# Kernel optimization log

Hardware: AMD Instinct MI355X
Metric: run time of the kernel (lower is better)

## Reference

```python
import jax, jax.numpy as jnp
import numpy as np

D_MODEL = 256
N_HEAD = 4
LEN_Q, LEN_K, BATCH = 1024, 4096, 8


def setup_inputs() -> dict:
    key = jax.random.key(0)
    ks = jax.random.split(key, 10)
    s = 0.02  # small init scale (stands in for xavier)
    return {
        "tgt": jax.random.normal(ks[0], (LEN_Q, BATCH, D_MODEL), jnp.float32),
        "memory": jax.random.normal(ks[1], (LEN_K, BATCH, D_MODEL), jnp.float32),
        "pos": jax.random.normal(ks[2], (LEN_K, BATCH, D_MODEL), jnp.float32),
        "query_pos": jax.random.normal(ks[3], (LEN_Q, BATCH, D_MODEL), jnp.float32),
        # nn.Linear weights, torch layout [out, in]
        "Wq": jax.random.normal(ks[4], (N_HEAD * D_MODEL, D_MODEL), jnp.float32) * s,
        "Wk": jax.random.normal(ks[5], (N_HEAD * D_MODEL, D_MODEL), jnp.float32) * s,
        "Wv": jax.random.normal(ks[6], (N_HEAD * D_MODEL, D_MODEL), jnp.float32) * s,
        "Wfc": jax.random.normal(ks[7], (D_MODEL, N_HEAD * D_MODEL), jnp.float32) * s,
        "ln_g": jnp.ones((D_MODEL,), jnp.float32),
        "ln_b": jnp.zeros((D_MODEL,), jnp.float32),
    }


def _layernorm(x, g, b, eps=1e-5):
    mu = jnp.mean(x, axis=-1, keepdims=True)
    var = jnp.mean(jnp.square(x - mu), axis=-1, keepdims=True)
    return (x - mu) * jax.lax.rsqrt(var + eps) * g + b


def reference(tgt, memory, pos, query_pos, Wq, Wk, Wv, Wfc, ln_g, ln_b):
    H, D = N_HEAD, D_MODEL
    # seq-first -> batch-first  [B, L, D]
    q = jnp.swapaxes(tgt + query_pos, 0, 1)
    k = jnp.swapaxes(memory + pos, 0, 1)
    v = jnp.swapaxes(memory, 0, 1)
    # per-head projections: each head has full d_model width
    Wq_h = Wq.reshape(H, D, D)
    Wk_h = Wk.reshape(H, D, D)
    Wv_h = Wv.reshape(H, D, D)
    qh = jnp.einsum('bqd,hed->bhqe', q, Wq_h)  # [B,H,Lq,D]
    kh = jnp.einsum('bkd,hed->bhke', k, Wk_h)  # [B,H,Lk,D]
    vh = jnp.einsum('bkd,hed->bhke', v, Wv_h)  # [B,H,Lk,D]
    scale = 1.0 / jnp.sqrt(jnp.asarray(D, qh.dtype))
    attn_logits = jnp.einsum('bhqe,bhke->bhqk', qh * scale, kh)  # [B,H,Lq,Lk]
    attn = jax.nn.softmax(attn_logits, axis=-1)
    out = jnp.einsum('bhqk,bhke->bhqe', attn, vh)  # [B,H,Lq,D]
    # mean logits across heads (keepdim), as returned attention map
    attn_mean = jnp.mean(attn_logits, axis=1, keepdims=True)  # [B,1,Lq,Lk]
    # concat heads, fc projection
    out = jnp.swapaxes(out, 1, 2).reshape(out.shape[0], -1, H * D)  # [B,Lq,H*D]
    out = out @ Wfc.T  # [B,Lq,D]
    tgt2 = jnp.swapaxes(out, 0, 1)  # back to [Lq,B,D]
    # residual + LayerNorm (dropout=0.0)
    y = _layernorm(tgt + tgt2, ln_g, ln_b)
    return (y, attn_mean)
```

## Files before the change

### kernel.cpp

```cpp
#include <hip/hip_runtime.h>
#include <cstdint>
#include <cstddef>

#define LQ 1024
#define LK 4096
#define NBATCH 8
#define DM 256
#define NH 4

typedef __attribute__((ext_vector_type(8))) __bf16 bf16x8;
typedef __attribute__((ext_vector_type(4))) float f32x4;
typedef __attribute__((ext_vector_type(4))) unsigned int u32x4;
typedef __attribute__((ext_vector_type(4))) short s16x4;

__device__ __forceinline__ unsigned short f2bf(float f) {
  unsigned int u = __builtin_bit_cast(unsigned int, f);
  u += 0x7FFFu + ((u >> 16) & 1u);
  return (unsigned short)(u >> 16);
}
__device__ __forceinline__ unsigned pack2(float a, float b) {
  return (unsigned)f2bf(a) | ((unsigned)f2bf(b) << 16);
}
__device__ __forceinline__ bf16x8 ld_bf8(const unsigned short* p) {
  u32x4 u = *reinterpret_cast<const u32x4*>(p);
  return __builtin_bit_cast(bf16x8, u);
}
__device__ __forceinline__ f32x4 zero4() {
  f32x4 v; v.x = 0.f; v.y = 0.f; v.z = 0.f; v.w = 0.f; return v;
}

#define ASYNC16(ldsp, gp)                                                      \
  __builtin_amdgcn_global_load_lds(                                            \
      (const __attribute__((address_space(1))) unsigned int*)(gp),             \
      (__attribute__((address_space(3))) unsigned int*)(ldsp), 16, 0, 0)

__global__ void prep_add_kernel(const float* __restrict__ a,
                                const float* __restrict__ badd,
                                unsigned short* __restrict__ out,
                                int L, int n8) {
  int i = blockIdx.x * blockDim.x + threadIdx.x;
  if (i >= n8) return;
  int base = i * 8;
  int d = base & 255;
  int rest = base >> 8;
  int bb = rest & 7, l = rest >> 3;
  f32x4 x0 = *reinterpret_cast<const f32x4*>(a + base);
  f32x4 x1 = *reinterpret_cast<const f32x4*>(a + base + 4);
  if (badd) {
    f32x4 y0 = *reinterpret_cast<const f32x4*>(badd + base);
    f32x4 y1 = *reinterpret_cast<const f32x4*>(badd + base + 4);
    x0 += y0; x1 += y1;
  }
  u32x4 o;
  o.x = pack2(x0.x, x0.y); o.y = pack2(x0.z, x0.w);
  o.z = pack2(x1.x, x1.y); o.w = pack2(x1.z, x1.w);
  *reinterpret_cast<u32x4*>(out + (((size_t)bb * L + l) << 8) + d) = o;
}

__global__ void conv_bf16_kernel(const float* __restrict__ src,
                                 unsigned short* __restrict__ dst, int n8) {
  int i = blockIdx.x * blockDim.x + threadIdx.x;
  if (i >= n8) return;
  int base = i * 8;
  f32x4 x0 = *reinterpret_cast<const f32x4*>(src + base);
  f32x4 x1 = *reinterpret_cast<const f32x4*>(src + base + 4);
  u32x4 o;
  o.x = pack2(x0.x, x0.y); o.y = pack2(x0.z, x0.w);
  o.z = pack2(x1.x, x1.y); o.w = pack2(x1.z, x1.w);
  *reinterpret_cast<u32x4*>(dst + base) = o;
}

template <int OUT_MODE>
__global__ void __launch_bounds__(256)
gemm_nt_kernel(const unsigned short* __restrict__ A, int lda, long long sA,
               const unsigned short* __restrict__ B, int ldb, long long sB,
               void* __restrict__ Cv, int ldc, long long sC,
               int K, float alpha) {
  __shared__ __align__(16) unsigned short As[128 * 64];
  __shared__ __align__(16) unsigned short Bs[128 * 64];
  const int t = threadIdx.x;
  const int bm0 = blockIdx.y * 128;
  const int bn0 = blockIdx.x * 128;
  A += (size_t)blockIdx.z * sA + (size_t)bm0 * lda;
  B += (size_t)blockIdx.z * sB + (size_t)bn0 * ldb;
  const int lane = t & 63, w = t >> 6;
  const int wm = (w >> 1) * 64, wn = (w & 1) * 64;
  const int lr = lane & 15, quad = lane >> 4;
  const int srl = lane >> 3;
  const int sc = (lane & 7) ^ (srl & 7);

  f32x4 acc[4][4];
#pragma unroll
  for (int i = 0; i < 4; ++i)
#pragma unroll
    for (int j = 0; j < 4; ++j) acc[i][j] = zero4();

  for (int k0 = 0; k0 < K; k0 += 64) {
#pragma unroll
    for (int i = 0; i < 4; ++i) {
      int r0 = w * 32 + i * 8;
      ASYNC16(&As[r0 * 64], &A[(size_t)(r0 + srl) * lda + k0 + sc * 8]);
      ASYNC16(&Bs[r0 * 64], &B[(size_t)(r0 + srl) * ldb + k0 + sc * 8]);
    }
    __syncthreads();
#pragma unroll
    for (int ks = 0; ks < 2; ++ks) {
      bf16x8 af[4], bfv[4];
#pragma unroll
      for (int i = 0; i < 4; ++i) {
        int m = wm + i * 16 + lr;
        int pc = (ks * 4 + quad) ^ (lr & 7);
        af[i] = ld_bf8(&As[m * 64 + pc * 8]);
      }
#pragma unroll
      for (int j = 0; j < 4; ++j) {
        int n = wn + j * 16 + lr;
        int pc = (ks * 4 + quad) ^ (lr & 7);
        bfv[j] = ld_bf8(&Bs[n * 64 + pc * 8]);
      }
#pragma unroll
      for (int i = 0; i < 4; ++i)
#pragma unroll
        for (int j = 0; j < 4; ++j)
          acc[i][j] = __builtin_amdgcn_mfma_f32_16x16x32_bf16(af[i], bfv[j], acc[i][j], 0, 0, 0);
    }
    __syncthreads();
  }

  if (OUT_MODE == 0) {
    float* C = (float*)Cv + (size_t)blockIdx.z * sC;
#pragma unroll
    for (int i = 0; i < 4; ++i) {
      int m0 = bm0 + wm + i * 16 + quad * 4;
#pragma unroll
      for (int j = 0; j < 4; ++j) {
        int n = bn0 + wn + j * 16 + lr;
#pragma unroll
        for (int r = 0; r < 4; ++r)
          C[(size_t)(m0 + r) * ldc + n] = acc[i][j][r] * alpha;
      }
    }
  } else if (OUT_MODE == 1) {
    unsigned short* C = (unsigned short*)Cv + (size_t)blockIdx.z * sC;
#pragma unroll
    for (int i = 0; i < 4; ++i) {
      int m0 = bm0 + wm + i * 16 + quad * 4;
#pragma unroll
      for (int j = 0; j < 4; ++j) {
        int n = bn0 + wn + j * 16 + lr;
#pragma unroll
        for (int r = 0; r < 4; ++r)
          C[(size_t)(m0 + r) * ldc + n] = f2bf(acc[i][j][r] * alpha);
      }
    }
  } else {
    unsigned short* C = (unsigned short*)Cv;
#pragma unroll
    for (int i = 0; i < 4; ++i) {
      int m0 = bm0 + wm + i * 16 + quad * 4;
      int bb = m0 >> 12;
      int kp = m0 & 4095;
#pragma unroll
      for (int j = 0; j < 4; ++j) {
        int n = bn0 + wn + j * 16 + lr;
        s16x4 pk;
#pragma unroll
        for (int r = 0; r < 4; ++r) pk[r] = (short)f2bf(acc[i][j][r] * alpha);
        *reinterpret_cast<s16x4*>(&C[((size_t)(bb * 1024 + n)) * 4096 + kp]) = pk;
      }
    }
  }
}

__global__ void __launch_bounds__(256, 2)
attn_kernel(const unsigned short* __restrict__ Qg,
            const unsigned short* __restrict__ Kg,
            const unsigned short* __restrict__ VTg,
            unsigned short* __restrict__ Opart,
            float* __restrict__ lpart) {
  __shared__ __align__(16) unsigned short Kt[2][32 * 256];
  __shared__ __align__(16) unsigned short Vt[2][256 * 32];
  const int t = threadIdx.x;
  const int qt = blockIdx.x >> 1, ks = blockIdx.x & 1;
  const int h = blockIdx.y, b = blockIdx.z;
  const int lane = t & 63, w = t >> 6;
  const int lr = lane & 15, quad = lane >> 4;

  const unsigned short* Qrow0 =
      Qg + ((size_t)(b * 1024 + qt * 128 + w * 32 + lr)) * 1024 + h * 256;
  bf16x8 qf[2][8];
#pragma unroll
  for (int s = 0; s < 8; ++s) {
    qf[0][s] = ld_bf8(&Qrow0[s * 32 + quad * 8]);
    qf[1][s] = ld_bf8(&Qrow0[16 * 1024 + s * 32 + quad * 8]);
  }

  f32x4 Oacc[16][2];
#pragma unroll
  for (int m2 = 0; m2 < 16; ++m2) {
    Oacc[m2][0] = zero4();
    Oacc[m2][1] = zero4();
  }
  float lsum_r[2] = {0.f, 0.f};

  const unsigned short* Kb =
      Kg + ((size_t)(b * 4096 + ks * 2048)) * 1024 + h * 256;
  const unsigned short* Vb =
      VTg + ((size_t)(b * 1024 + h * 256)) * 4096 + ks * 2048;

  const int k_rsub = lane >> 5;
  const int k_chunk = lane & 31;
  const int v_rsub = lane >> 2;
  const int v_chunk = lane & 3;

#define ISSUE_TILE(kt, bufsel)                                                 \
  {                                                                            \
    _Pragma("unroll") for (int i = 0; i < 4; ++i) {                            \
      int r0 = w * 8 + i * 2;                                                  \
      int krow = r0 + k_rsub;                                                  \
      int kc = k_chunk ^ (krow & 7);                                           \
      ASYNC16(&Kt[bufsel][r0 * 256], &Kb[(size_t)((kt) + krow) * 1024 + kc * 8]); \
      int vr0 = (w * 4 + i) * 16;                                              \
      int ve = vr0 + v_rsub;                                                   \
      int vc = v_chunk ^ ((ve >> 1) & 3);                                      \
      ASYNC16(&Vt[bufsel][vr0 * 32], &Vb[(size_t)ve * 4096 + (kt) + vc * 8]);  \
    }                                                                          \
  }

  ISSUE_TILE(0, 0)
  __syncthreads();

  const int bpermA = (((quad & 1) * 32) + lr) * 4;
  const int bpermB = bpermA + 64;

  for (int kt = 0; kt < 2048; kt += 32) {
    const int pbuf = (kt >> 5) & 1;
    ISSUE_TILE(kt + 32, pbuf ^ 1)

    const unsigned short* Ktp = Kt[pbuf];
    const unsigned short* Vtp = Vt[pbuf];

    f32x4 S[2][2];
    S[0][0] = zero4(); S[0][1] = zero4();
    S[1][0] = zero4(); S[1][1] = zero4();
#pragma unroll
    for (int s = 0; s < 8; ++s) {
      int pc = ((s * 4 + quad) ^ (lr & 7)) * 8;
      bf16x8 kf0 = ld_bf8(&Ktp[lr * 256 + pc]);
      bf16x8 kf1 = ld_bf8(&Ktp[(16 + lr) * 256 + pc]);
      S[0][0] = __builtin_amdgcn_mfma_f32_16x16x32_bf16(kf0, qf[0][s], S[0][0], 0, 0, 0);
      S[0][1] = __builtin_amdgcn_mfma_f32_16x16x32_bf16(kf0, qf[1][s], S[0][1], 0, 0, 0);
      S[1][0] = __builtin_amdgcn_mfma_f32_16x16x32_bf16(kf1, qf[0][s], S[1][0], 0, 0, 0);
      S[1][1] = __builtin_amdgcn_mfma_f32_16x16x32_bf16(kf1, qf[1][s], S[1][1], 0, 0, 0);
    }

    unsigned pk[2][2][2];
#pragma unroll
    for (int mt = 0; mt < 2; ++mt)
#pragma unroll
      for (int nt = 0; nt < 2; ++nt) {
        float p0 = __expf(S[mt][nt][0]);
        float p1 = __expf(S[mt][nt][1]);
        float p2 = __expf(S[mt][nt][2]);
        float p3 = __expf(S[mt][nt][3]);
        lsum_r[nt] += (p0 + p1) + (p2 + p3);
        pk[mt][nt][0] = pack2(p0, p1);
        pk[mt][nt][1] = pack2(p2, p3);
      }

    bf16x8 pfrag[2];
#pragma unroll
    for (int nt = 0; nt < 2; ++nt) {
      u32x4 bfw;
#pragma unroll
      for (int w2 = 0; w2 < 2; ++w2) {
        int f0 = __builtin_amdgcn_ds_bpermute(bpermA, (int)pk[0][nt][w2]);
        int f1 = __builtin_amdgcn_ds_bpermute(bpermA, (int)pk[1][nt][w2]);
        bfw[w2] = (unsigned)(quad < 2 ? f0 : f1);
        int g0 = __builtin_amdgcn_ds_bpermute(bpermB, (int)pk[0][nt][w2]);
        int g1 = __builtin_amdgcn_ds_bpermute(bpermB, (int)pk[1][nt][w2]);
        bfw[2 + w2] = (unsigned)(quad < 2 ? g0 : g1);
      }
      pfrag[nt] = __builtin_bit_cast(bf16x8, bfw);
    }

#pragma unroll
    for (int m2 = 0; m2 < 16; ++m2) {
      bf16x8 vf = ld_bf8(&Vtp[(m2 * 16 + lr) * 32 + (quad ^ ((lr >> 1) & 3)) * 8]);
      Oacc[m2][0] = __builtin_amdgcn_mfma_f32_16x16x32_bf16(vf, pfrag[0], Oacc[m2][0], 0, 0, 0);
      Oacc[m2][1] = __builtin_amdgcn_mfma_f32_16x16x32_bf16(vf, pfrag[1], Oacc[m2][1], 0, 0, 0);
    }
    __syncthreads();
  }
#undef ISSUE_TILE

  const int pidx = b * 4 + h;
#pragma unroll
  for (int nt = 0; nt < 2; ++nt) {
    float l = lsum_r[nt];
    l += __shfl_xor(l, 16, 64);
    l += __shfl_xor(l, 32, 64);
    if (quad == 0)
      lpart[((size_t)(ks * 32 + pidx)) * 1024 + qt * 128 + w * 32 + nt * 16 + lr] = l;
  }

  const size_t base = ((size_t)(ks * 32 + pidx)) * 256 * 1024;
  const int qg0 = qt * 128 + w * 32 + lr;
#pragma unroll
  for (int m2 = 0; m2 < 16; ++m2) {
#pragma unroll
    for (int nt = 0; nt < 2; ++nt) {
#pragma unroll
      for (int r = 0; r < 4; ++r) {
        int e = m2 * 16 + quad * 4 + r;
        Opart[base + (size_t)e * 1024 + qg0 + nt * 16] = f2bf(Oacc[m2][nt][r]);
      }
    }
  }
}

__global__ void __launch_bounds__(256)
combine_kernel(const unsigned short* __restrict__ Opart,
               const float* __restrict__ lpart,
               unsigned short* __restrict__ Oall) {
  __shared__ float rl[64];
  __shared__ __align__(16) unsigned short T[64][264];
  const int t = threadIdx.x;
  const int qt = blockIdx.x, h = blockIdx.y, b = blockIdx.z;
  const int p = b * 4 + h;
  const int q0 = qt * 64;
  const size_t slabO = (size_t)32 * 256 * 1024;
  const size_t slabL = (size_t)32 * 1024;
  if (t < 64) {
    float la = lpart[(size_t)p * 1024 + q0 + t];
    float lb = lpart[slabL + (size_t)p * 1024 + q0 + t];
    rl[t] = 1.f / (la + lb);
  }
  __syncthreads();
  const int er = t >> 3, q8 = t & 7;
#pragma unroll
  for (int ei = 0; ei < 8; ++ei) {
    int e = ei * 32 + er;
    size_t idx = ((size_t)p * 256 + e) * 1024 + q0 + q8 * 8;
    u32x4 ua = *reinterpret_cast<const u32x4*>(&Opart[idx]);
    u32x4 ub = *reinterpret_cast<const u32x4*>(&Opart[slabO + idx]);
#pragma unroll
    for (int wd = 0; wd < 4; ++wd) {
      unsigned a = ((const unsigned*)&ua)[wd], bb2 = ((const unsigned*)&ub)[wd];
      float a0 = __builtin_bit_cast(float, a << 16);
      float a1 = __builtin_bit_cast(float, a & 0xFFFF0000u);
      float b0 = __builtin_bit_cast(float, bb2 << 16);
      float b1 = __builtin_bit_cast(float, bb2 & 0xFFFF0000u);
      int qA = q8 * 8 + wd * 2;
      T[qA + 0][e] = f2bf((a0 + b0) * rl[qA + 0]);
      T[qA + 1][e] = f2bf((a1 + b1) * rl[qA + 1]);
    }
  }
  __syncthreads();
  const int ql = t >> 2, ec = t & 3;
  const size_t orow = ((size_t)(b * 1024 + q0 + ql)) * 1024 + h * 256;
#pragma unroll
  for (int i = 0; i < 8; ++i) {
    int ch = ec * 8 + i;
    *reinterpret_cast<u32x4*>(&Oall[orow + ch * 8]) =
        *reinterpret_cast<const u32x4*>(&T[ql][ch * 8]);
  }
}

__global__ void __launch_bounds__(256)
fc_ln_kernel(const float* __restrict__ fc, const float* __restrict__ tgt,
             const float* __restrict__ g, const float* __restrict__ bb,
             float* __restrict__ y) {
  int row = blockIdx.x * 4 + (threadIdx.x >> 6);
  int lane = threadIdx.x & 63;
  int b = row >> 10, q = row & 1023;
  const float* fr = fc + (size_t)row * 256;
  const float* tr = tgt + ((size_t)(q * 8 + b)) * 256;
  float x[4];
  float s = 0.f, ss = 0.f;
#pragma unroll
  for (int e = 0; e < 4; ++e) {
    x[e] = fr[lane + e * 64] + tr[lane + e * 64];
    s += x[e];
    ss += x[e] * x[e];
  }
#pragma unroll
  for (int d = 1; d < 64; d <<= 1) {
    s += __shfl_xor(s, d, 64);
    ss += __shfl_xor(ss, d, 64);
  }
  float mu = s * (1.f / 256.f);
  float var = ss * (1.f / 256.f) - mu * mu;
  float rs = rsqrtf(var + 1e-5f);
  float* yr = y + ((size_t)(q * 8 + b)) * 256;
#pragma unroll
  for (int e = 0; e < 4; ++e)
    yr[lane + e * 64] = (x[e] - mu) * rs * g[lane + e * 64] + bb[lane + e * 64];
}

extern "C" void kernel_launch(void* const* d_in, const int* in_sizes, int n_in,
                              void* d_out, int out_size, void* d_ws, size_t ws_size,
                              hipStream_t stream) {
  (void)in_sizes; (void)n_in; (void)out_size; (void)ws_size;
  const float* tgt    = (const float*)d_in[0];
  const float* memory = (const float*)d_in[1];
  const float* pos    = (const float*)d_in[2];
  const float* qpos   = (const float*)d_in[3];
  const float* Wq     = (const float*)d_in[4];
  const float* Wk     = (const float*)d_in[5];
  const float* Wv     = (const float*)d_in[6];
  const float* Wfc    = (const float*)d_in[7];
  const float* lng    = (const float*)d_in[8];
  const float* lnb    = (const float*)d_in[9];
  float* out = (float*)d_out;

  char* ws = (char*)d_ws;
  const size_t MB = 1024 * 1024;
  unsigned short* Wq_b  = (unsigned short*)(ws + 0);
  unsigned short* Wk_b  = (unsigned short*)(ws + 512 * 1024);
  unsigned short* Wv_b  = (unsigned short*)(ws + 1 * MB);
  unsigned short* Wfc_b = (unsigned short*)(ws + 1 * MB + 512 * 1024);
  unsigned short* A_q   = (unsigned short*)(ws + 2 * MB);
  unsigned short* A_k   = (unsigned short*)(ws + 6 * MB);
  unsigned short* A_v   = (unsigned short*)(ws + 22 * MB);
  unsigned short* Qall  = (unsigned short*)(ws + 38 * MB);
  unsigned short* Kall  = (unsigned short*)(ws + 54 * MB);
  unsigned short* VTb   = (unsigned short*)(ws + 118 * MB);
  unsigned short* Opart = (unsigned short*)(ws + 2 * MB);
  float* lpart          = (float*)(ws + 36 * MB);
  unsigned short* Oall  = (unsigned short*)(ws + 118 * MB);
  float* fcout          = (float*)(ws + 140 * MB);
  float* y = out;
  float* attn_mean = out + (size_t)LQ * NBATCH * DM;

  int n_q = LQ * NBATCH * DM;
  int n_k = LK * NBATCH * DM;
  prep_add_kernel<<<(n_q / 8 + 255) / 256, 256, 0, stream>>>(tgt, qpos, A_q, LQ, n_q / 8);
  prep_add_kernel<<<(n_k / 8 + 255) / 256, 256, 0, stream>>>(memory, pos, A_k, LK, n_k / 8);
  prep_add_kernel<<<(n_k / 8 + 255) / 256, 256, 0, stream>>>(memory, nullptr, A_v, LK, n_k / 8);
  int n_w8 = 1024 * 256 / 8;
  conv_bf16_kernel<<<(n_w8 + 255) / 256, 256, 0, stream>>>(Wq, Wq_b, n_w8);
  conv_bf16_kernel<<<(n_w8 + 255) / 256, 256, 0, stream>>>(Wk, Wk_b, n_w8);
  conv_bf16_kernel<<<(n_w8 + 255) / 256, 256, 0, stream>>>(Wv, Wv_b, n_w8);
  conv_bf16_kernel<<<(n_w8 + 255) / 256, 256, 0, stream>>>(Wfc, Wfc_b, n_w8);

  gemm_nt_kernel<1><<<dim3(8, 64, 1), 256, 0, stream>>>(
      A_q, 256, 0LL, Wq_b, 256, 0LL, (void*)Qall, 1024, 0LL, 256, 0.0625f);
  gemm_nt_kernel<1><<<dim3(8, 256, 1), 256, 0, stream>>>(
      A_k, 256, 0LL, Wk_b, 256, 0LL, (void*)Kall, 1024, 0LL, 256, 1.0f);
  gemm_nt_kernel<2><<<dim3(8, 256, 1), 256, 0, stream>>>(
      A_v, 256, 0LL, Wv_b, 256, 0LL, (void*)VTb, 0, 0LL, 256, 1.0f);
  gemm_nt_kernel<0><<<dim3(32, 8, 8), 256, 0, stream>>>(
      Qall, 1024, (long long)(1024 * 1024), Kall, 1024, (long long)(4096 * 1024),
      (void*)attn_mean, 4096, (long long)4096 * 1024, 1024, 0.25f);
  attn_kernel<<<dim3(16, NH, NBATCH), 256, 0, stream>>>(Qall, Kall, VTb, Opart, lpart);
  combine_kernel<<<dim3(16, NH, NBATCH), 256, 0, stream>>>(Opart, lpart, Oall);
  gemm_nt_kernel<0><<<dim3(2, 64, 1), 256, 0, stream>>>(
      Oall, 1024, 0LL, Wfc_b, 1024, 0LL, (void*)fcout, 256, 0LL, 1024, 1.0f);
  fc_ln_kernel<<<2048, 256, 0, stream>>>(fcout, tgt, lng, lnb, y);
}
```

Before: 650.9 us.

## Halve attention query tile, single-buffer V, remap blocks to XCDs, add setprio

Each attention block now handles 64 query rows instead of 128 (one 16-row fragment per wave), which cuts the Q-fragment and O-accumulator registers and raises launch bounds to 3 blocks per CU. V is single-buffered in LDS to save shared memory, loaded after an extra barrier at the end of each iteration. The grid is flattened to 1024 blocks, remapped so that blocks sharing a (batch, head, key-split) run on the same XCD for L2 reuse of K/V, and s_setprio is raised around the MFMA sections. The cost is twice as many K/V tile reads per query, an additional __syncthreads per iteration, and V loads that are no longer overlapped with compute.

```diff
diff --git a/kernel.cpp b/kernel.cpp
--- a/kernel.cpp
+++ b/kernel.cpp
@@ -172,36 +172,35 @@
   }
 }
 
-__global__ void __launch_bounds__(256, 2)
+__global__ void __launch_bounds__(256, 3)
 attn_kernel(const unsigned short* __restrict__ Qg,
             const unsigned short* __restrict__ Kg,
             const unsigned short* __restrict__ VTg,
             unsigned short* __restrict__ Opart,
             float* __restrict__ lpart) {
   __shared__ __align__(16) unsigned short Kt[2][32 * 256];
-  __shared__ __align__(16) unsigned short Vt[2][256 * 32];
+  __shared__ __align__(16) unsigned short Vt[256 * 32];
   const int t = threadIdx.x;
-  const int qt = blockIdx.x >> 1, ks = blockIdx.x & 1;
-  const int h = blockIdx.y, b = blockIdx.z;
+  const int lin = blockIdx.x;
+  const int xcd = lin & 7;
+  const int blk = lin >> 3;
+  const int qt = blk & 15;
+  const int shi = blk >> 4;
+  const int s_id = xcd + 8 * shi;
+  const int ks = s_id & 1, h = (s_id >> 1) & 3, b = s_id >> 3;
   const int lane = t & 63, w = t >> 6;
   const int lr = lane & 15, quad = lane >> 4;
 
   const unsigned short* Qrow0 =
-      Qg + ((size_t)(b * 1024 + qt * 128 + w * 32 + lr)) * 1024 + h * 256;
-  bf16x8 qf[2][8];
-#pragma unroll
-  for (int s = 0; s < 8; ++s) {
-    qf[0][s] = ld_bf8(&Qrow0[s * 32 + quad * 8]);
-    qf[1][s] = ld_bf8(&Qrow0[16 * 1024 + s * 32 + quad * 8]);
-  }
-
-  f32x4 Oacc[16][2];
-#pragma unroll
-  for (int m2 = 0; m2 < 16; ++m2) {
-    Oacc[m2][0] = zero4();
-    Oacc[m2][1] = zero4();
-  }
-  float lsum_r[2] = {0.f, 0.f};
+      Qg + ((size_t)(b * 1024 + qt * 64 + w * 16 + lr)) * 1024 + h * 256;
+  bf16x8 qf[8];
+#pragma unroll
+  for (int s = 0; s < 8; ++s) qf[s] = ld_bf8(&Qrow0[s * 32 + quad * 8]);
+
+  f32x4 Oacc[16];
+#pragma unroll
+  for (int m2 = 0; m2 < 16; ++m2) Oacc[m2] = zero4();
+  float lsum_r = 0.f;
 
   const unsigned short* Kb =
       Kg + ((size_t)(b * 4096 + ks * 2048)) * 1024 + h * 256;
@@ -213,108 +212,107 @@
   const int v_rsub = lane >> 2;
   const int v_chunk = lane & 3;
 
-#define ISSUE_TILE(kt, bufsel)                                                 \
+#define ISSUE_K(kt, bufsel)                                                    \
   {                                                                            \
     _Pragma("unroll") for (int i = 0; i < 4; ++i) {                            \
       int r0 = w * 8 + i * 2;                                                  \
       int krow = r0 + k_rsub;                                                  \
       int kc = k_chunk ^ (krow & 7);                                           \
       ASYNC16(&Kt[bufsel][r0 * 256], &Kb[(size_t)((kt) + krow) * 1024 + kc * 8]); \
+    }                                                                          \
+  }
+#define ISSUE_V(kt)                                                            \
+  {                                                                            \
+    _Pragma("unroll") for (int i = 0; i < 4; ++i) {                            \
       int vr0 = (w * 4 + i) * 16;                                              \
       int ve = vr0 + v_rsub;                                                   \
       int vc = v_chunk ^ ((ve >> 1) & 3);                                      \
-      ASYNC16(&Vt[bufsel][vr0 * 32], &Vb[(size_t)ve * 4096 + (kt) + vc * 8]);  \
+      ASYNC16(&Vt[vr0 * 32], &Vb[(size_t)ve * 4096 + (kt) + vc * 8]);          \
     }                                                                          \
   }
 
-  ISSUE_TILE(0, 0)
+  ISSUE_K(0, 0)
+  ISSUE_V(0)
   __syncthreads();
 
   const int bpermA = (((quad & 1) * 32) + lr) * 4;
   const int bpermB = bpermA + 64;
 
   for (int kt = 0; kt < 2048; kt += 32) {
-    const int pbuf = (kt >> 5) & 1;
-    ISSUE_TILE(kt + 32, pbuf ^ 1)
-
-    const unsigned short* Ktp = Kt[pbuf];
-    const unsigned short* Vtp = Vt[pbuf];
-
-    f32x4 S[2][2];
-    S[0][0] = zero4(); S[0][1] = zero4();
-    S[1][0] = zero4(); S[1][1] = zero4();
+    const int pb = (kt >> 5) & 1;
+    ISSUE_K(kt + 32, pb ^ 1)
+
+    const unsigned short* Ktp = Kt[pb];
+
+    f32x4 S[2];
+    S[0] = zero4(); S[1] = zero4();
+    __builtin_amdgcn_s_setprio(1);
 #pragma unroll
     for (int s = 0; s < 8; ++s) {
       int pc = ((s * 4 + quad) ^ (lr & 7)) * 8;
       bf16x8 kf0 = ld_bf8(&Ktp[lr * 256 + pc]);
       bf16x8 kf1 = ld_bf8(&Ktp[(16 + lr) * 256 + pc]);
-      S[0][0] = __builtin_amdgcn_mfma_f32_16x16x32_bf16(kf0, qf[0][s], S[0][0], 0, 0, 0);
-      S[0][1] = __builtin_amdgcn_mfma_f32_16x16x32_bf16(kf0, qf[1][s], S[0][1], 0, 0, 0);
-      S[1][0] = __builtin_amdgcn_mfma_f32_16x16x32_bf16(kf1, qf[0][s], S[1][0], 0, 0, 0);
-      S[1][1] = __builtin_amdgcn_mfma_f32_16x16x32_bf16(kf1, qf[1][s], S[1][1], 0, 0, 0);
-    }
-
-    unsigned pk[2][2][2];
-#pragma unroll
-    for (int mt = 0; mt < 2; ++mt)
-#pragma unroll
-      for (int nt = 0; nt < 2; ++nt) {
-        float p0 = __expf(S[mt][nt][0]);
-        float p1 = __expf(S[mt][nt][1]);
-        float p2 = __expf(S[mt][nt][2]);
-        float p3 = __expf(S[mt][nt][3]);
-        lsum_r[nt] += (p0 + p1) + (p2 + p3);
-        pk[mt][nt][0] = pack2(p0, p1);
-        pk[mt][nt][1] = pack2(p2, p3);
-      }
-
-    bf16x8 pfrag[2];
-#pragma unroll
-    for (int nt = 0; nt < 2; ++nt) {
-      u32x4 bfw;
-#pragma unroll
-      for (int w2 = 0; w2 < 2; ++w2) {
-        int f0 = __builtin_amdgcn_ds_bpermute(bpermA, (int)pk[0][nt][w2]);
-        int f1 = __builtin_amdgcn_ds_bpermute(bpermA, (int)pk[1][nt][w2]);
-        bfw[w2] = (unsigned)(quad < 2 ? f0 : f1);
-        int g0 = __builtin_amdgcn_ds_bpermute(bpermB, (int)pk[0][nt][w2]);
-        int g1 = __builtin_amdgcn_ds_bpermute(bpermB, (int)pk[1][nt][w2]);
-        bfw[2 + w2] = (unsigned)(quad < 2 ? g0 : g1);
-      }
-      pfrag[nt] = __builtin_bit_cast(bf16x8, bfw);
-    }
-
+      S[0] = __builtin_amdgcn_mfma_f32_16x16x32_bf16(kf0, qf[s], S[0], 0, 0, 0);
+      S[1] = __builtin_amdgcn_mfma_f32_16x16x32_bf16(kf1, qf[s], S[1], 0, 0, 0);
+    }
+    __builtin_amdgcn_s_setprio(0);
+
+    unsigned pk[2][2];
+#pragma unroll
+    for (int mt = 0; mt < 2; ++mt) {
+      float p0 = __expf(S[mt][0]);
+      float p1 = __expf(S[mt][1]);
+      float p2 = __expf(S[mt][2]);
+      float p3 = __expf(S[mt][3]);
+      lsum_r += (p0 + p1) + (p2 + p3);
+      pk[mt][0] = pack2(p0, p1);
+      pk[mt][1] = pack2(p2, p3);
+    }
+
+    u32x4 bfw;
+#pragma unroll
+    for (int w2 = 0; w2 < 2; ++w2) {
+      int f0 = __builtin_amdgcn_ds_bpermute(bpermA, (int)pk[0][w2]);
+      int f1 = __builtin_amdgcn_ds_bpermute(bpermA, (int)pk[1][w2]);
+      bfw[w2] = (unsigned)(quad < 2 ? f0 : f1);
+      int g0 = __builtin_amdgcn_ds_bpermute(bpermB, (int)pk[0][w2]);
+      int g1 = __builtin_amdgcn_ds_bpermute(bpermB, (int)pk[1][w2]);
+      bfw[2 + w2] = (unsigned)(quad < 2 ? g0 : g1);
+    }
+    bf16x8 pfrag = __builtin_bit_cast(bf16x8, bfw);
+
+    __builtin_amdgcn_s_setprio(1);
 #pragma unroll
     for (int m2 = 0; m2 < 16; ++m2) {
-      bf16x8 vf = ld_bf8(&Vtp[(m2 * 16 + lr) * 32 + (quad ^ ((lr >> 1) & 3)) * 8]);
-      Oacc[m2][0] = __builtin_amdgcn_mfma_f32_16x16x32_bf16(vf, pfrag[0], Oacc[m2][0], 0, 0, 0);
-      Oacc[m2][1] = __builtin_amdgcn_mfma_f32_16x16x32_bf16(vf, pfrag[1], Oacc[m2][1], 0, 0, 0);
-    }
+      bf16x8 vf = ld_bf8(&Vt[(m2 * 16 + lr) * 32 + (quad ^ ((lr >> 1) & 3)) * 8]);
+      Oacc[m2] = __builtin_amdgcn_mfma_f32_16x16x32_bf16(vf, pfrag, Oacc[m2], 0, 0, 0);
+    }
+    __builtin_amdgcn_s_setprio(0);
+
     __syncthreads();
-  }
-#undef ISSUE_TILE
+    ISSUE_V(kt + 32)
+    __syncthreads();
+  }
+#undef ISSUE_K
+#undef ISSUE_V
 
   const int pidx = b * 4 + h;
-#pragma unroll
-  for (int nt = 0; nt < 2; ++nt) {
-    float l = lsum_r[nt];
+  {
+    float l = lsum_r;
     l += __shfl_xor(l, 16, 64);
     l += __shfl_xor(l, 32, 64);
     if (quad == 0)
-      lpart[((size_t)(ks * 32 + pidx)) * 1024 + qt * 128 + w * 32 + nt * 16 + lr] = l;
+      lpart[((size_t)(ks * 32 + pidx)) * 1024 + qt * 64 + w * 16 + lr] = l;
   }
 
   const size_t base = ((size_t)(ks * 32 + pidx)) * 256 * 1024;
-  const int qg0 = qt * 128 + w * 32 + lr;
+  const int qg0 = qt * 64 + w * 16 + lr;
 #pragma unroll
   for (int m2 = 0; m2 < 16; ++m2) {
 #pragma unroll
-    for (int nt = 0; nt < 2; ++nt) {
-#pragma unroll
-      for (int r = 0; r < 4; ++r) {
-        int e = m2 * 16 + quad * 4 + r;
-        Opart[base + (size_t)e * 1024 + qg0 + nt * 16] = f2bf(Oacc[m2][nt][r]);
-      }
+    for (int r = 0; r < 4; ++r) {
+      int e = m2 * 16 + quad * 4 + r;
+      Opart[base + (size_t)e * 1024 + qg0] = f2bf(Oacc[m2][r]);
     }
   }
 }
@@ -453,7 +451,7 @@
   gemm_nt_kernel<0><<<dim3(32, 8, 8), 256, 0, stream>>>(
       Qall, 1024, (long long)(1024 * 1024), Kall, 1024, (long long)(4096 * 1024),
       (void*)attn_mean, 4096, (long long)4096 * 1024, 1024, 0.25f);
-  attn_kernel<<<dim3(16, NH, NBATCH), 256, 0, stream>>>(Qall, Kall, VTb, Opart, lpart);
+  attn_kernel<<<dim3(1024, 1, 1), 256, 0, stream>>>(Qall, Kall, VTb, Opart, lpart);
   combine_kernel<<<dim3(16, NH, NBATCH), 256, 0, stream>>>(Opart, lpart, Oall);
   gemm_nt_kernel<0><<<dim3(2, 64, 1), 256, 0, stream>>>(
       Oall, 1024, 0LL, Wfc_b, 1024, 0LL, (void*)fcout, 256, 0LL, 1024, 1.0f);
```

Measured after the change: 723.4 us. +11.1%, slower.

## Compute mean attention logits via folded Wk^T·Wq Gram matrix with K=256

Applied to the files above, without the earlier changes.

The head-averaged logits are computed by precomputing G = sum_h Wk_h^T Wq_h / (H·sqrt(D)), projecting queries through G, and multiplying against the unprojected keys. This cuts the reduction dimension of the large Lq×Lk logits GEMM from 1024 to 256, reducing its FLOPs roughly fourfold. The cost is a weight transpose, a small Gram GEMM and one extra Lq×256 projection. It also adds a different bf16 rounding path for the averaged logits.

```diff
diff --git a/kernel.cpp b/kernel.cpp
--- a/kernel.cpp
+++ b/kernel.cpp
@@ -68,6 +68,25 @@
   o.x = pack2(x0.x, x0.y); o.y = pack2(x0.z, x0.w);
   o.z = pack2(x1.x, x1.y); o.w = pack2(x1.z, x1.w);
   *reinterpret_cast<u32x4*>(dst + base) = o;
+}
+
+__global__ void __launch_bounds__(256)
+transpose_w_kernel(const float* __restrict__ in, unsigned short* __restrict__ out) {
+  __shared__ float ts[64][65];
+  const int t = threadIdx.x;
+  const int he0 = blockIdx.x * 64, d0 = blockIdx.y * 64;
+  const int rh = t >> 6, c = t & 63;
+#pragma unroll
+  for (int i = 0; i < 16; ++i) {
+    int r = i * 4 + rh;
+    ts[r][c] = in[(size_t)(he0 + r) * 256 + d0 + c];
+  }
+  __syncthreads();
+#pragma unroll
+  for (int i = 0; i < 16; ++i) {
+    int r = i * 4 + rh;
+    out[(size_t)(d0 + r) * 1024 + he0 + c] = f2bf(ts[c][r]);
+  }
 }
 
 template <int OUT_MODE>
@@ -423,7 +442,11 @@
   unsigned short* A_q   = (unsigned short*)(ws + 2 * MB);
   unsigned short* A_k   = (unsigned short*)(ws + 6 * MB);
   unsigned short* A_v   = (unsigned short*)(ws + 22 * MB);
+  unsigned short* Tq    = (unsigned short*)(ws + 22 * MB);
   unsigned short* Qall  = (unsigned short*)(ws + 38 * MB);
+  unsigned short* WqT   = (unsigned short*)(ws + 38 * MB);
+  unsigned short* WkT   = (unsigned short*)(ws + 38 * MB + 512 * 1024);
+  unsigned short* GT    = (unsigned short*)(ws + 39 * MB);
   unsigned short* Kall  = (unsigned short*)(ws + 54 * MB);
   unsigned short* VTb   = (unsigned short*)(ws + 118 * MB);
   unsigned short* Opart = (unsigned short*)(ws + 2 * MB);
@@ -435,10 +458,21 @@
 
   int n_q = LQ * NBATCH * DM;
   int n_k = LK * NBATCH * DM;
+  int n_w8 = 1024 * 256 / 8;
+
+  transpose_w_kernel<<<dim3(16, 4), 256, 0, stream>>>(Wq, WqT);
+  transpose_w_kernel<<<dim3(16, 4), 256, 0, stream>>>(Wk, WkT);
+  gemm_nt_kernel<1><<<dim3(2, 2, 1), 256, 0, stream>>>(
+      WkT, 1024, 0LL, WqT, 1024, 0LL, (void*)GT, 256, 0LL, 1024, 0.015625f);
   prep_add_kernel<<<(n_q / 8 + 255) / 256, 256, 0, stream>>>(tgt, qpos, A_q, LQ, n_q / 8);
   prep_add_kernel<<<(n_k / 8 + 255) / 256, 256, 0, stream>>>(memory, pos, A_k, LK, n_k / 8);
+  gemm_nt_kernel<1><<<dim3(2, 64, 1), 256, 0, stream>>>(
+      A_q, 256, 0LL, GT, 256, 0LL, (void*)Tq, 256, 0LL, 256, 1.0f);
+  gemm_nt_kernel<0><<<dim3(32, 8, 8), 256, 0, stream>>>(
+      Tq, 256, (long long)(1024 * 256), A_k, 256, (long long)(4096 * 256),
+      (void*)attn_mean, 4096, (long long)4096 * 1024, 256, 1.0f);
+
   prep_add_kernel<<<(n_k / 8 + 255) / 256, 256, 0, stream>>>(memory, nullptr, A_v, LK, n_k / 8);
-  int n_w8 = 1024 * 256 / 8;
   conv_bf16_kernel<<<(n_w8 + 255) / 256, 256, 0, stream>>>(Wq, Wq_b, n_w8);
   conv_bf16_kernel<<<(n_w8 + 255) / 256, 256, 0, stream>>>(Wk, Wk_b, n_w8);
   conv_bf16_kernel<<<(n_w8 + 255) / 256, 256, 0, stream>>>(Wv, Wv_b, n_w8);
@@ -450,9 +484,7 @@
       A_k, 256, 0LL, Wk_b, 256, 0LL, (void*)Kall, 1024, 0LL, 256, 1.0f);
   gemm_nt_kernel<2><<<dim3(8, 256, 1), 256, 0, stream>>>(
       A_v, 256, 0LL, Wv_b, 256, 0LL, (void*)VTb, 0, 0LL, 256, 1.0f);
-  gemm_nt_kernel<0><<<dim3(32, 8, 8), 256, 0, stream>>>(
-      Qall, 1024, (long long)(1024 * 1024), Kall, 1024, (long long)(4096 * 1024),
-      (void*)attn_mean, 4096, (long long)4096 * 1024, 1024, 0.25f);
+
   attn_kernel<<<dim3(16, NH, NBATCH), 256, 0, stream>>>(Qall, Kall, VTb, Opart, lpart);
   combine_kernel<<<dim3(16, NH, NBATCH), 256, 0, stream>>>(Opart, lpart, Oall);
   gemm_nt_kernel<0><<<dim3(2, 64, 1), 256, 0, stream>>>(
```

New measurement: 588.8 us. 1.11x faster.
